# Kernel tuning notes

Hardware: AMD Instinct MI355X
Metric: run time of the kernel (lower is better)

## Reference

```python
import jax, jax.numpy as jnp
import numpy as np

EPS = 1e-8
CG_TOL = 1e-4
S_SIGMA = 8   # bilateral grid spatial downsampling
N_BINS = 9    # bilateral grid range bins (intensity in [0,1])


def _conv2d(x, k):
    # x [C,H,W], k [kh,kw] -> same-padded cross-correlation, per channel
    kh, kw = k.shape
    out = jax.lax.conv_general_dilated(x[:, None], k[None, None], (1, 1),
                                       [(kh // 2, kh // 2), (kw // 2, kw // 2)])
    return out[:, 0]


def _conv2d_T(x, k):
    return _conv2d(x, k[::-1, ::-1])


def _conv_bank(x, ks):
    # x [C,H,W], ks [N,kh,kw] -> [N,C,H,W]
    n, kh, kw = ks.shape
    out = jax.lax.conv_general_dilated(x[:, None], ks[:, None], (1, 1),
                                       [(kh // 2, kh // 2), (kw // 2, kw // 2)])
    return out.transpose(1, 0, 2, 3)


def _conv_bank_T(v, ks):
    # v [N,C,H,W] -> sum_n conv(v[n], flip(ks[n])) : [C,H,W]
    n, kh, kw = ks.shape
    lhs = v.transpose(1, 0, 2, 3)          # [C,N,H,W]
    rhs = ks[:, ::-1, ::-1][None]          # [1,N,kh,kw]
    out = jax.lax.conv_general_dilated(lhs, rhs, (1, 1),
                                       [(kh // 2, kh // 2), (kw // 2, kw // 2)])
    return out[:, 0]


def _deconv_grad(blurred, x, kernel, dkw, dks, rkw, rks, rpow, reg_targets):
    # gradient of E(x) = sum_i dkw_i ||dk_i * (k*x - b)||^2
    #                  + sum_j rkw_j sum |rk_j*x - t_j|^{p_j}
    Kx = _conv2d(x, kernel) - blurred
    d = _conv_bank(Kx, dks)                                    # [Nd,C,H,W]
    g = _conv2d_T(_conv_bank_T(2.0 * dkw[:, None, None, None] * d, dks), kernel)
    v = _conv_bank(x, rks) - reg_targets                       # [Nr,C,H,W]
    av = jnp.abs(v) + EPS
    phi = jnp.sign(v) * av ** (rpow[:, None, None, None] - 1.0)
    g = g + _conv_bank_T(rkw[:, None, None, None] * rpow[:, None, None, None] * phi, rks)
    return g


def _deconv_alpha(blurred, x, kernel, dkw, dks, rkw, rks, rpow, reg_targets, p):
    # exact line search for the quadratic part, Gauss-Newton for |.|^p prior
    g = _deconv_grad(blurred, x, kernel, dkw, dks, rkw, rks, rpow, reg_targets)
    num = -jnp.sum(g * p)
    Kp = _conv2d(p, kernel)
    dKp = _conv_bank(Kp, dks)
    den = jnp.sum(2.0 * dkw[:, None, None, None] * dKp ** 2)
    v = _conv_bank(x, rks) - reg_targets
    Rp = _conv_bank(p, rks)
    w = (rkw * rpow * (rpow - 1.0))[:, None, None, None]
    den = den + jnp.sum(w * (jnp.abs(v) + EPS) ** (rpow[:, None, None, None] - 2.0) * Rp ** 2)
    return num / (den + 1e-12)


def _deconv_prior(x, rks, thr):
    # soft-shrinkage of filtered responses -> regularization targets
    v = _conv_bank(x, rks)
    return jnp.sign(v) * jnp.maximum(jnp.abs(v) - thr[:, None, None, None], 0.0)


def _conv_axis(g, f, axis):
    k = f.shape[0]; r = k // 2; L = g.shape[axis]
    pad = [(0, 0)] * g.ndim; pad[axis] = (r, r)
    gp = jnp.pad(g, pad)
    out = jnp.zeros_like(g)
    for t in range(k):  # fixed small tap count
        out = out + f[t] * jax.lax.slice_in_dim(gp, t, t + L, axis=axis)
    return out


def _bilateral_channel(I, fs, fr):
    # learned-filter bilateral grid: splat -> separable filter (fs,fs,fr) -> trilinear slice
    H, W = I.shape
    gh, gw = H // S_SIGMA, W // S_SIGMA
    Ic = jnp.clip(I, 0.0, 1.0)
    yy, xx = jnp.meshgrid(jnp.arange(H), jnp.arange(W), indexing="ij")
    yi = yy // S_SIGMA; xi = xx // S_SIGMA
    zi = jnp.clip(jnp.round(Ic * (N_BINS - 1)).astype(jnp.int32), 0, N_BINS - 1)
    flat = ((yi * gw + xi) * N_BINS + zi).ravel()
    gv = jnp.zeros(gh * gw * N_BINS, Ic.dtype).at[flat].add(Ic.ravel())
    gw_ = jnp.zeros(gh * gw * N_BINS, Ic.dtype).at[flat].add(1.0)
    g2 = jnp.stack([gv, gw_], -1).reshape(gh, gw, N_BINS, 2)
    g2 = _conv_axis(_conv_axis(_conv_axis(g2, fs, 0), fs, 1), fr, 2)
    yf = yy / S_SIGMA; xf = xx / S_SIGMA; zf = Ic * (N_BINS - 1)

    def corners(f, n):
        c0 = jnp.clip(jnp.floor(f).astype(jnp.int32), 0, n - 1)
        c1 = jnp.minimum(c0 + 1, n - 1)
        w = jnp.clip(f - c0, 0.0, 1.0)
        return c0, c1, w

    y0, y1, wy = corners(yf, gh)
    x0, x1, wx = corners(xf, gw)
    z0, z1, wz = corners(zf, N_BINS)
    acc = jnp.zeros(I.shape + (2,), Ic.dtype)
    for yc, wyc in ((y0, 1 - wy), (y1, wy)):
        for xc, wxc in ((x0, 1 - wx), (x1, wx)):
            for zc, wzc in ((z0, 1 - wz), (z1, wz)):
                acc = acc + (wyc * wxc * wzc)[..., None] * g2[yc, xc, zc]
    return acc[..., 0] / (acc[..., 1] + 1e-8)


def _forward(blurred_batch, kernel_batch, data_kernels, data_kernel_weights,
             reg_kernels, reg_kernel_weights, reg_powers, filter_s, filter_r,
             reg_thresholds, num_cg_iter):
    num_stages = filter_s.shape[0]
    n_reg = reg_kernels.shape[1]

    def single(blurred, kernel):
        def cg(x, idx, reg_targets):
            dkw = data_kernel_weights[idx]; dks = data_kernels[idx]
            rkw = reg_kernel_weights[idx]; rks = reg_kernels[idx]; rp = reg_powers[idx]
            g = _deconv_grad(blurred, x, kernel, dkw, dks, rkw, rks, rp, reg_targets)
            r = -g
            r_norm = jnp.sum(r * r)
            r0 = r_norm

            def body(i, carry):
                x, r, p, rn, done = carry
                alpha = _deconv_alpha(blurred, x, kernel, dkw, dks, rkw, rks, rp, reg_targets, p)
                x1 = x + alpha * p
                g1 = _deconv_grad(blurred, x1, kernel, dkw, dks, rkw, rks, rp, reg_targets)
                r1 = -g1
                nrn = jnp.sum(r1 * r1)
                beta = nrn / (rn + 1e-20)
                conv_now = nrn < CG_TOL * r0
                p1 = r1 + beta * p
                x_n = jnp.where(done, x, x1)
                r_n = jnp.where(done, r, r1)
                rn_n = jnp.where(done, rn, nrn)
                p_n = jnp.where(done | conv_now, p, p1)
                return (x_n, r_n, p_n, rn_n, done | conv_now)

            carry = (x, r, r, r_norm, jnp.array(False))
            x, _, _, _, _ = jax.lax.fori_loop(0, num_cg_iter, body, carry)
            return x

        x = cg(blurred, 0, jnp.zeros((n_reg,) + blurred.shape, blurred.dtype))
        for stage in range(num_stages):
            x = jax.vmap(lambda ch: _bilateral_channel(ch, filter_s[stage], filter_r[stage]))(x)
            reg_targets = _deconv_prior(x, reg_kernels[stage + 1], reg_thresholds[stage])
            x = cg(x, stage + 1, reg_targets)
        return x

    return jax.vmap(single)(blurred_batch, kernel_batch)


def setup_inputs() -> dict:
    key = jax.random.key(0)
    k1, k2 = jax.random.split(key)
    B, C, H, W, KS = 2, 3, 512, 512, 15
    blurred = jax.random.uniform(k1, (B, C, H, W), jnp.float32)
    kern = jax.random.uniform(k2, (B, KS, KS), jnp.float32)
    kern = kern / jnp.sum(kern, axis=(1, 2), keepdims=True)  # normalized PSFs

    ns = 1; c = 2  # num_stages, kernel center (5x5)
    rk = np.zeros((ns + 1, 5, 5, 5), np.float32)
    rk[:, 0, c, c] = -1.0; rk[:, 0, c + 1, c] = 1.0
    rk[:, 1, c, c] = -1.0; rk[:, 1, c, c + 1] = 1.0
    rk[:, 2, c, c] = 1.0; rk[:, 2, c + 1, c] = -1.0
    rk[:, 2, c, c + 1] = -1.0; rk[:, 2, c + 1, c + 1] = 1.0
    rk[:, 3, c - 1, c] = 1.0; rk[:, 3, c, c] = -2.0; rk[:, 3, c + 1, c] = 1.0
    rk[:, 4, c, c - 1] = 1.0; rk[:, 4, c, c] = -2.0; rk[:, 4, c, c + 1] = 1.0
    dk = np.zeros((ns + 1, 6, 5, 5), np.float32)
    dk[:, 0, c, c] = 1.0
    dk[:, 1:] = rk
    dkw = np.zeros((ns + 1, 6), np.float32); dkw[:, 0] = 1.0
    rkw = np.zeros((ns + 1, 5), np.float32)
    rkw[0, :] = 0.001; rkw[1:, :] = 0.05
    rpow = np.full((ns + 1, 5), 2.0, np.float32)
    fs = np.zeros((ns, 11), np.float32); fs[:, 3:8] = [0.0, 1.0, 2.0, 1.0, 0.0]
    fr = np.tile(np.array([0.0, 1.0, 2.0, 1.0, 0.0], np.float32), (ns, 1))
    thr = np.tile(np.array([0.065, 0.065, 0.0325, 0.0325, 0.0325], np.float32), (ns, 1))

    return {
        "blurred_batch": blurred,
        "kernel_batch": kern,
        "data_kernels": jnp.asarray(dk),
        "data_kernel_weights": jnp.asarray(dkw),
        "reg_kernels": jnp.asarray(rk),
        "reg_kernel_weights": jnp.asarray(rkw),
        "reg_powers": jnp.asarray(rpow),
        "filter_s": jnp.asarray(fs),
        "filter_r": jnp.asarray(fr),
        "reg_thresholds": jnp.asarray(thr),
        "num_cg_iter": 5,
    }


def reference(blurred_batch, kernel_batch, data_kernels, data_kernel_weights,
              reg_kernels, reg_kernel_weights, reg_powers, filter_s, filter_r,
              reg_thresholds, num_cg_iter):
    return _forward(blurred_batch, kernel_batch, data_kernels, data_kernel_weights,
                    reg_kernels, reg_kernel_weights, reg_powers, filter_s, filter_r,
                    reg_thresholds, num_cg_iter)
```

## Files before the change

kernel.cpp:

```cpp
#include <hip/hip_runtime.h>

constexpr int Bn = 2, Cn = 3, Hh = 512, Ww = 512;
constexpr int KS = 15, KR = 7;
constexpr int NDK = 6, NRK = 5;
constexpr int GH = 64, GW = 64, NBn = 9, SS = 8;
constexpr float EPSf = 1e-8f;
constexpr float CGTOL = 1e-4f;
constexpr int PLANE = Hh * Ww;
constexpr int CHW = Cn * PLANE;
constexpr int BX = 64, BY = 16;
constexpr int GXc = Ww / BX, GYc = Hh / BY;
constexpr int PB = GXc * GYc * Cn;
constexpr int SA = 80, THt = 30;
constexpr int S2W = 72, S2H = 24;
constexpr int PHW = 68, PHH = 20;
constexpr int PHG = (PHW / 4) * PHH;
constexpr int NITER = 5;

struct CgState { float alpha, beta, rn, r0; int done, pflag; int pad0, pad1; };

__device__ __forceinline__ float blockReduce(float v, float* red, int tid) {
    red[tid] = v; __syncthreads();
    for (int s = 128; s > 0; s >>= 1) { if (tid < s) red[tid] += red[tid + s]; __syncthreads(); }
    float r = red[0]; __syncthreads();
    return r;
}

__global__ __launch_bounds__(256)
void k_conv15(const float* __restrict__ src, const float* __restrict__ rb,
              const float* __restrict__ pbuf, float* __restrict__ xcopy,
              const float* __restrict__ sub, float* __restrict__ out,
              const float* __restrict__ kernB, float* __restrict__ part,
              const CgState* __restrict__ st, const int* __restrict__ ncg,
              int iter, int mode)
{
    const int pz = blockIdx.z, b = pz / Cn, c = pz % Cn;
    const CgState s = st[b];
    if (mode == 2 && (s.done != 0 || iter >= *ncg)) return;
    __shared__ __align__(16) float tile[SA * THt];
    __shared__ __align__(16) float kkp[15 * 16];
    __shared__ float red[256];
    const int tx = threadIdx.x, ty = threadIdx.y, tid = ty * 16 + tx;
    const int ox0 = blockIdx.x * BX, oy0 = blockIdx.y * BY;
    const int baseP = pz * PLANE;
    const float beta = s.beta; const int pf = s.pflag;

    const float* kp = kernB + b * 225;
    for (int i = tid; i < 225; i += 256) kkp[(i / 15) * 16 + (i % 15)] = kp[i];

    float nm = 0.f;
    for (int i = tid; i < 78 * THt; i += 256) {
        int ly = i / 78, lx = i % 78;
        int gy = oy0 - KR + ly, gx = ox0 - KR + lx;
        float v = 0.f;
        if (gy >= 0 && gy < Hh && gx >= 0 && gx < Ww) {
            int gi = baseP + gy * Ww + gx;
            if (mode == 2) {
                float rv = rb[gi], pv = pbuf[gi];
                v = pf ? fmaf(beta, pv, rv) : pv;
                if (ly >= KR && ly < KR + BY && lx >= KR && lx < KR + BX)
                    nm = fmaf(rv, v, nm);
            } else {
                v = src[gi];
                if (mode == 0 && ly >= KR && ly < KR + BY && lx >= KR && lx < KR + BX)
                    xcopy[gi] = v;
            }
        }
        tile[ly * SA + lx] = v;
    }
    __syncthreads();

    const int colbase = tx * 4;
    float a0 = 0.f, a1 = 0.f, a2 = 0.f, a3 = 0.f;
    for (int i = 0; i < KS; i++) {
        const float4* rp4 = reinterpret_cast<const float4*>(&tile[(ty + i) * SA + colbase]);
        float f[20];
        #pragma unroll
        for (int s5 = 0; s5 < 5; s5++) {
            float4 w4 = rp4[s5];
            f[s5 * 4] = w4.x; f[s5 * 4 + 1] = w4.y; f[s5 * 4 + 2] = w4.z; f[s5 * 4 + 3] = w4.w;
        }
        const float4* kr4 = reinterpret_cast<const float4*>(&kkp[i * 16]);
        float kf[16];
        #pragma unroll
        for (int s5 = 0; s5 < 4; s5++) {
            float4 k4 = kr4[s5];
            kf[s5 * 4] = k4.x; kf[s5 * 4 + 1] = k4.y; kf[s5 * 4 + 2] = k4.z; kf[s5 * 4 + 3] = k4.w;
        }
        #pragma unroll
        for (int j = 0; j < KS; j++) {
            float kv = kf[j];
            a0 = fmaf(kv, f[j], a0); a1 = fmaf(kv, f[j + 1], a1);
            a2 = fmaf(kv, f[j + 2], a2); a3 = fmaf(kv, f[j + 3], a3);
        }
    }
    const int gi = baseP + (oy0 + ty) * Ww + ox0 + colbase;
    if (sub) {
        float4 sv = *reinterpret_cast<const float4*>(&sub[gi]);
        a0 -= sv.x; a1 -= sv.y; a2 -= sv.z; a3 -= sv.w;
    }
    *reinterpret_cast<float4*>(&out[gi]) = make_float4(a0, a1, a2, a3);
    if (mode == 2) {
        float tot = blockReduce(nm, red, tid);
        if (tid == 0) {
            int blk = c * (GXc * GYc) + blockIdx.y * GXc + blockIdx.x;
            part[((size_t)b * 4 + 0) * PB + blk] = tot;
        }
    }
}

__global__ __launch_bounds__(256)
void k_bank(const float* __restrict__ sbuf, float* __restrict__ tbuf,
            const float* __restrict__ dks, const float* __restrict__ dkw,
            const CgState* __restrict__ st, const int* __restrict__ ncg,
            int iter, int mode)
{
    const int pz = blockIdx.z, b = pz / Cn;
    if (mode == 1 && (st[b].done != 0 || iter >= *ncg)) return;
    __shared__ __align__(16) float sl[S2W * S2H];
    __shared__ __align__(16) float dl[PHW * PHH];
    __shared__ float dkk[NDK * 25];
    __shared__ float dww[NDK];
    const int tx = threadIdx.x, ty = threadIdx.y, tid = ty * 16 + tx;
    const int ox0 = blockIdx.x * BX, oy0 = blockIdx.y * BY;
    const int baseP = pz * PLANE;
    const int colbase = tx * 4;
    for (int i = tid; i < NDK * 25; i += 256) dkk[i] = dks[i];
    if (tid < NDK) dww[tid] = dkw[tid];
    __syncthreads();

    bool fast = true;
    for (int n = 0; n < NDK; n++) {
        if (dww[n] == 0.f) continue;
        int nnz = 0;
        for (int q = 0; q < 25; q++) if (dkk[n * 25 + q] != 0.f) nnz++;
        if (nnz > 1) fast = false;
    }

    if (fast) {
        const int gy = oy0 + ty, gx0 = ox0 + colbase;
        const float4 sv = *reinterpret_cast<const float4*>(&sbuf[baseP + gy * Ww + gx0]);
        float o0 = 0.f, o1 = 0.f, o2 = 0.f, o3 = 0.f;
        for (int n = 0; n < NDK; n++) {
            float wn = 2.f * dww[n];
            if (wn == 0.f) continue;
            int pa = -1, pb = 0; float pv = 0.f;
            for (int q = 0; q < 25; q++) {
                float vq = dkk[n * 25 + q];
                if (vq != 0.f) { pa = q / 5; pb = q % 5; pv = vq; }
            }
            if (pa < 0) continue;
            int dy = pa - 2, dx = pb - 2;
            float sc = wn * pv * pv;
            if ((gy - dy) < 0 || (gy - dy) >= Hh) continue;
            if ((gx0     - dx) >= 0 && (gx0     - dx) < Ww) o0 = fmaf(sc, sv.x, o0);
            if ((gx0 + 1 - dx) >= 0 && (gx0 + 1 - dx) < Ww) o1 = fmaf(sc, sv.y, o1);
            if ((gx0 + 2 - dx) >= 0 && (gx0 + 2 - dx) < Ww) o2 = fmaf(sc, sv.z, o2);
            if ((gx0 + 3 - dx) >= 0 && (gx0 + 3 - dx) < Ww) o3 = fmaf(sc, sv.w, o3);
        }
        *reinterpret_cast<float4*>(&tbuf[baseP + gy * Ww + gx0]) = make_float4(o0, o1, o2, o3);
        return;
    }

    for (int i = tid; i < S2W * S2H; i += 256) {
        int ly = i / S2W, lx = i % S2W;
        int gy = oy0 - 4 + ly, gx = ox0 - 4 + lx;
        sl[i] = (gy >= 0 && gy < Hh && gx >= 0 && gx < Ww) ? sbuf[baseP + gy * Ww + gx] : 0.f;
    }
    __syncthreads();
    float t0 = 0.f, t1 = 0.f, t2 = 0.f, t3 = 0.f;
    for (int n = 0; n < NDK; n++) {
        float wn = 2.f * dww[n];
        if (wn == 0.f) continue;
        float dnr[25];
        #pragma unroll
        for (int q = 0; q < 25; q++) dnr[q] = dkk[n * 25 + q];
        for (int t = tid; t < PHG; t += 256) {
            int zy = t / 17, zx0 = (t % 17) * 4;
            int gy = oy0 - 2 + zy, gx0 = ox0 - 2 + zx0;
            float v0 = 0.f, v1 = 0.f, v2 = 0.f, v3 = 0.f;
            #pragma unroll
            for (int a = 0; a < 5; a++) {
                bool rz = dnr[a*5]==0.f && dnr[a*5+1]==0.f && dnr[a*5+2]==0.f &&
                          dnr[a*5+3]==0.f && dnr[a*5+4]==0.f;
                if (rz) continue;
                const float4* s4 = reinterpret_cast<const float4*>(&sl[(zy + a) * S2W + zx0]);
                float4 u0 = s4[0], u1 = s4[1];
                float f8[8] = {u0.x,u0.y,u0.z,u0.w,u1.x,u1.y,u1.z,u1.w};
                #pragma unroll
                for (int bb = 0; bb < 5; bb++) {
                    float kv = dnr[a * 5 + bb];
                    if (kv != 0.f) {
                        v0 = fmaf(kv, f8[bb], v0); v1 = fmaf(kv, f8[bb+1], v1);
                        v2 = fmaf(kv, f8[bb+2], v2); v3 = fmaf(kv, f8[bb+3], v3);
                    }
                }
            }
            bool gyin = (gy >= 0 && gy < Hh);
            if (!gyin || gx0     < 0 || gx0     >= Ww) v0 = 0.f;
            if (!gyin || gx0 + 1 < 0 || gx0 + 1 >= Ww) v1 = 0.f;
            if (!gyin || gx0 + 2 < 0 || gx0 + 2 >= Ww) v2 = 0.f;
            if (!gyin || gx0 + 3 < 0 || gx0 + 3 >= Ww) v3 = 0.f;
            *reinterpret_cast<float4*>(&dl[zy * PHW + zx0]) = make_float4(v0, v1, v2, v3);
        }
        __syncthreads();
        float c0 = 0.f, c1 = 0.f, c2 = 0.f, c3 = 0.f;
        #pragma unroll
        for (int a = 0; a < 5; a++) {
            int fr = 4 - a;
            bool rz = dnr[fr*5]==0.f && dnr[fr*5+1]==0.f && dnr[fr*5+2]==0.f &&
                      dnr[fr*5+3]==0.f && dnr[fr*5+4]==0.f;
            if (rz) continue;
            const float4* q4 = reinterpret_cast<const float4*>(&dl[(ty + a) * PHW + colbase]);
            float4 u0 = q4[0], u1 = q4[1];
            float f8[8] = {u0.x,u0.y,u0.z,u0.w,u1.x,u1.y,u1.z,u1.w};
            #pragma unroll
            for (int bb = 0; bb < 5; bb++) {
                float kv = dnr[fr * 5 + (4 - bb)];
                if (kv != 0.f) {
                    c0 = fmaf(kv, f8[bb], c0); c1 = fmaf(kv, f8[bb+1], c1);
                    c2 = fmaf(kv, f8[bb+2], c2); c3 = fmaf(kv, f8[bb+3], c3);
                }
            }
        }
        t0 = fmaf(wn, c0, t0); t1 = fmaf(wn, c1, t1);
        t2 = fmaf(wn, c2, t2); t3 = fmaf(wn, c3, t3);
        __syncthreads();
    }
    const int gi = baseP + (oy0 + ty) * Ww + ox0 + colbase;
    *reinterpret_cast<float4*>(&tbuf[gi]) = make_float4(t0, t1, t2, t3);
}

__global__ __launch_bounds__(256)
void k_grad(const float* __restrict__ wbuf, const float* __restrict__ xg,
            const float* __restrict__ rb, const float* __restrict__ pbuf,
            const float* __restrict__ tgt, float* __restrict__ outb,
            float* __restrict__ pout, const float* __restrict__ kernB,
            const float* __restrict__ rks, const float* __restrict__ rkw,
            const float* __restrict__ rpw, float* __restrict__ part,
            const CgState* __restrict__ st, const int* __restrict__ ncg,
            int iter, int mode)
{
    const int pz = blockIdx.z, b = pz / Cn, c = pz % Cn;
    const CgState s = st[b];
    if (mode == 1 && (s.done != 0 || iter >= *ncg)) return;
    __shared__ __align__(16) float wt[SA * THt];
    __shared__ __align__(16) float s2[S2W * S2H];
    __shared__ __align__(16) float ph[PHW * PHH];
    __shared__ __align__(16) float kkp[15 * 16];
    __shared__ float rk5[NRK * 25];
    __shared__ float srkw[NRK], srpw[NRK];
    __shared__ float red[256];
    const int tx = threadIdx.x, ty = threadIdx.y, tid = ty * 16 + tx;
    const int ox0 = blockIdx.x * BX, oy0 = blockIdx.y * BY;
    const int baseP = pz * PLANE;
    const float beta = s.beta; const int pf = s.pflag;

    const float* kp = kernB + b * 225;
    for (int i = tid; i < 225; i += 256) kkp[(i / 15) * 16 + (i % 15)] = kp[224 - i];
    for (int i = tid; i < NRK * 25; i += 256) rk5[i] = rks[i];
    if (tid < NRK) { srkw[tid] = rkw[tid]; srpw[tid] = rpw[tid]; }

    for (int i = tid; i < 78 * THt; i += 256) {
        int ly = i / 78, lx = i % 78;
        int gy = oy0 - KR + ly, gx = ox0 - KR + lx;
        wt[ly * SA + lx] = (gy >= 0 && gy < Hh && gx >= 0 && gx < Ww)
                           ? wbuf[baseP + gy * Ww + gx] : 0.f;
    }
    for (int i = tid; i < S2W * S2H; i += 256) {
        int ly = i / S2W, lx = i % S2W;
        int gy = oy0 - 4 + ly, gx = ox0 - 4 + lx;
        float v = 0.f;
        if (gy >= 0 && gy < Hh && gx >= 0 && gx < Ww) {
            int gi = baseP + gy * Ww + gx;
            if (mode == 0) v = xg[gi];
            else { float rv = rb[gi], pv = pbuf[gi]; v = pf ? fmaf(beta, pv, rv) : pv; }
        }
        s2[i] = v;
    }
    __syncthreads();

    const int colbase = tx * 4;
    float a0 = 0.f, a1 = 0.f, a2 = 0.f, a3 = 0.f;
    for (int i = 0; i < KS; i++) {
        const float4* rp4 = reinterpret_cast<const float4*>(&wt[(ty + i) * SA + colbase]);
        float f[20];
        #pragma unroll
        for (int s5 = 0; s5 < 5; s5++) {
            float4 w4 = rp4[s5];
            f[s5 * 4] = w4.x; f[s5 * 4 + 1] = w4.y; f[s5 * 4 + 2] = w4.z; f[s5 * 4 + 3] = w4.w;
        }
        const float4* kr4 = reinterpret_cast<const float4*>(&kkp[i * 16]);
        float kf[16];
        #pragma unroll
        for (int s5 = 0; s5 < 4; s5++) {
            float4 k4 = kr4[s5];
            kf[s5 * 4] = k4.x; kf[s5 * 4 + 1] = k4.y; kf[s5 * 4 + 2] = k4.z; kf[s5 * 4 + 3] = k4.w;
        }
        #pragma unroll
        for (int j = 0; j < KS; j++) {
            float kv = kf[j];
            a0 = fmaf(kv, f[j], a0); a1 = fmaf(kv, f[j + 1], a1);
            a2 = fmaf(kv, f[j + 2], a2); a3 = fmaf(kv, f[j + 3], a3);
        }
    }

    for (int m = 0; m < NRK; m++) {
        float wm = srkw[m], rp = srpw[m];
        if (wm == 0.f) continue;
        float rmr[25];
        #pragma unroll
        for (int q = 0; q < 25; q++) rmr[q] = rk5[m * 25 + q];
        const float* tgm = tgt ? tgt + ((size_t)(b * NRK + m)) * CHW + (size_t)c * PLANE : nullptr;
        const float coefG = wm * rp;
        const float coefH = wm * rp * (rp - 1.f);

        for (int t = tid; t < PHG; t += 256) {
            int zy = t / 17, zx0 = (t % 17) * 4;
            int gy = oy0 - 2 + zy, gx0 = ox0 - 2 + zx0;
            float v0 = 0.f, v1 = 0.f, v2 = 0.f, v3 = 0.f;
            #pragma unroll
            for (int a = 0; a < 5; a++) {
                bool rz = rmr[a*5]==0.f && rmr[a*5+1]==0.f && rmr[a*5+2]==0.f &&
                          rmr[a*5+3]==0.f && rmr[a*5+4]==0.f;
                if (rz) continue;
                const float4* s4 = reinterpret_cast<const float4*>(&s2[(zy + a) * S2W + zx0]);
                float4 u0 = s4[0], u1 = s4[1];
                float f8[8] = {u0.x,u0.y,u0.z,u0.w,u1.x,u1.y,u1.z,u1.w};
                #pragma unroll
                for (int bb = 0; bb < 5; bb++) {
                    float kv = rmr[a * 5 + bb];
                    if (kv != 0.f) {
                        v0 = fmaf(kv, f8[bb], v0); v1 = fmaf(kv, f8[bb+1], v1);
                        v2 = fmaf(kv, f8[bb+2], v2); v3 = fmaf(kv, f8[bb+3], v3);
                    }
                }
            }
            bool gyin = (gy >= 0 && gy < Hh);
            float o0 = 0.f, o1 = 0.f, o2 = 0.f, o3 = 0.f;
            if (mode == 0) {
                if (gyin && gx0     >= 0 && gx0     < Ww) {
                    float v = v0; if (tgm) v -= tgm[gy * Ww + gx0];
                    float sg = (v > 0.f) ? 1.f : ((v < 0.f) ? -1.f : 0.f);
                    float av = fabsf(v) + EPSf;
                    o0 = coefG * sg * ((rp == 2.f) ? av : powf(av, rp - 1.f));
                }
                if (gyin && gx0 + 1 >= 0 && gx0 + 1 < Ww) {
                    float v = v1; if (tgm) v -= tgm[gy * Ww + gx0 + 1];
                    float sg = (v > 0.f) ? 1.f : ((v < 0.f) ? -1.f : 0.f);
                    float av = fabsf(v) + EPSf;
                    o1 = coefG * sg * ((rp == 2.f) ? av : powf(av, rp - 1.f));
                }
                if (gyin && gx0 + 2 >= 0 && gx0 + 2 < Ww) {
                    float v = v2; if (tgm) v -= tgm[gy * Ww + gx0 + 2];
                    float sg = (v > 0.f) ? 1.f : ((v < 0.f) ? -1.f : 0.f);
                    float av = fabsf(v) + EPSf;
                    o2 = coefG * sg * ((rp == 2.f) ? av : powf(av, rp - 1.f));
                }
                if (gyin && gx0 + 3 >= 0 && gx0 + 3 < Ww) {
                    float v = v3; if (tgm) v -= tgm[gy * Ww + gx0 + 3];
                    float sg = (v > 0.f) ? 1.f : ((v < 0.f) ? -1.f : 0.f);
                    float av = fabsf(v) + EPSf;
                    o3 = coefG * sg * ((rp == 2.f) ? av : powf(av, rp - 1.f));
                }
            } else {
                #pragma unroll
                for (int j = 0; j < 4; j++) {
                    int gx = gx0 + j;
                    if (!gyin || gx < 0 || gx >= Ww) continue;
                    float v = (j == 0) ? v0 : (j == 1) ? v1 : (j == 2) ? v2 : v3;
                    float fac = 1.f;
                    if (rp != 2.f) {
                        float vx = 0.f;
                        for (int a = 0; a < 5; a++)
                            for (int bb = 0; bb < 5; bb++) {
                                int yy = gy - 2 + a, xx = gx - 2 + bb;
                                if (yy >= 0 && yy < Hh && xx >= 0 && xx < Ww)
                                    vx = fmaf(rmr[a * 5 + bb], xg[baseP + yy * Ww + xx], vx);
                            }
                        if (tgm) vx -= tgm[gy * Ww + gx];
                        fac = powf(fabsf(vx) + EPSf, rp - 2.f);
                    }
                    float o = coefH * fac * v;
                    if (j == 0) o0 = o; else if (j == 1) o1 = o; else if (j == 2) o2 = o; else o3 = o;
                }
            }
            *reinterpret_cast<float4*>(&ph[zy * PHW + zx0]) = make_float4(o0, o1, o2, o3);
        }
        __syncthreads();
        #pragma unroll
        for (int a = 0; a < 5; a++) {
            int fr = 4 - a;
            bool rz = rmr[fr*5]==0.f && rmr[fr*5+1]==0.f && rmr[fr*5+2]==0.f &&
                      rmr[fr*5+3]==0.f && rmr[fr*5+4]==0.f;
            if (rz) continue;
            const float4* q4 = reinterpret_cast<const float4*>(&ph[(ty + a) * PHW + colbase]);
            float4 u0 = q4[0], u1 = q4[1];
            float f8[8] = {u0.x,u0.y,u0.z,u0.w,u1.x,u1.y,u1.z,u1.w};
            #pragma unroll
            for (int bb = 0; bb < 5; bb++) {
                float kv = rmr[fr * 5 + (4 - bb)];
                if (kv != 0.f) {
                    a0 = fmaf(kv, f8[bb], a0); a1 = fmaf(kv, f8[bb+1], a1);
                    a2 = fmaf(kv, f8[bb+2], a2); a3 = fmaf(kv, f8[bb+3], a3);
                }
            }
        }
        __syncthreads();
    }

    const int gi = baseP + (oy0 + ty) * Ww + ox0 + colbase;
    float redv;
    if (mode == 0) {
        float r0v = -a0, r1v = -a1, r2v = -a2, r3v = -a3;
        float4 rv4 = make_float4(r0v, r1v, r2v, r3v);
        *reinterpret_cast<float4*>(&outb[gi]) = rv4;
        *reinterpret_cast<float4*>(&pout[gi]) = rv4;
        redv = r0v * r0v + r1v * r1v + r2v * r2v + r3v * r3v;
    } else {
        *reinterpret_cast<float4*>(&outb[gi]) = make_float4(a0, a1, a2, a3);
        int li = (ty + 4) * S2W + colbase + 4;
        redv = s2[li] * a0 + s2[li + 1] * a1 + s2[li + 2] * a2 + s2[li + 3] * a3;
    }
    float tot = blockReduce(redv, red, tid);
    if (tid == 0) {
        int blk = c * (GXc * GYc) + blockIdx.y * GXc + blockIdx.x;
        int slot = (mode == 0) ? 2 : 1;
        part[((size_t)b * 4 + slot) * PB + blk] = tot;
    }
}

__global__ __launch_bounds__(256)
void k_axpy(float4* __restrict__ x, float4* __restrict__ r, float4* __restrict__ p,
            const float4* __restrict__ q, float* __restrict__ part,
            const CgState* __restrict__ st, const int* __restrict__ ncg, int iter)
{
    const int b = blockIdx.y;
    const CgState s = st[b];
    if (s.done != 0 || iter >= *ncg) return;
    __shared__ float red[256];
    const int tid = threadIdx.x;
    const int idx = b * (CHW / 4) + blockIdx.x * 256 + tid;
    float4 pv = p[idx], rv = r[idx], qv = q[idx], xv = x[idx];
    float4 pc;
    if (s.pflag) {
        pc.x = fmaf(s.beta, pv.x, rv.x); pc.y = fmaf(s.beta, pv.y, rv.y);
        pc.z = fmaf(s.beta, pv.z, rv.z); pc.w = fmaf(s.beta, pv.w, rv.w);
    } else pc = pv;
    xv.x = fmaf(s.alpha, pc.x, xv.x); xv.y = fmaf(s.alpha, pc.y, xv.y);
    xv.z = fmaf(s.alpha, pc.z, xv.z); xv.w = fmaf(s.alpha, pc.w, xv.w);
    rv.x = fmaf(-s.alpha, qv.x, rv.x); rv.y = fmaf(-s.alpha, qv.y, rv.y);
    rv.z = fmaf(-s.alpha, qv.z, rv.z); rv.w = fmaf(-s.alpha, qv.w, rv.w);
    x[idx] = xv; r[idx] = rv; p[idx] = pc;
    float nr = rv.x * rv.x + rv.y * rv.y + rv.z * rv.z + rv.w * rv.w;
    float tot = blockReduce(nr, red, tid);
    if (tid == 0) part[((size_t)b * 4 + 2) * PB + blockIdx.x] = tot;
}

__global__ __launch_bounds__(256)
void k_fin_alpha(const float* __restrict__ part, CgState* st,
                 const int* __restrict__ ncg, int iter)
{
    const int b = blockIdx.x, tid = threadIdx.x;
    __shared__ float red[256];
    if (st[b].done != 0 || iter >= *ncg) { if (tid == 0) st[b].alpha = 0.f; return; }
    float sn = 0.f, sd = 0.f;
    for (int i = tid; i < PB; i += 256) {
        sn += part[((size_t)b * 4 + 0) * PB + i];
        sd += part[((size_t)b * 4 + 1) * PB + i];
    }
    float num = blockReduce(sn, red, tid);
    float den = blockReduce(sd, red, tid);
    if (tid == 0) st[b].alpha = num / (den + 1e-12f);
}

__global__ __launch_bounds__(256)
void k_fin_iter(const float* __restrict__ part, CgState* st,
                const int* __restrict__ ncg, int iter, int mode)
{
    const int b = blockIdx.x, tid = threadIdx.x;
    __shared__ float red[256];
    if (mode == 1 && (st[b].done != 0 || iter >= *ncg)) { if (tid == 0) st[b].pflag = 0; return; }
    float s = 0.f;
    for (int i = tid; i < PB; i += 256) s += part[((size_t)b * 4 + 2) * PB + i];
    float nrn = blockReduce(s, red, tid);
    if (tid == 0) {
        if (mode == 0) {
            st[b].rn = nrn; st[b].r0 = nrn; st[b].done = 0; st[b].pflag = 0;
            st[b].beta = 0.f; st[b].alpha = 0.f;
        } else {
            float beta = nrn / (st[b].rn + 1e-20f);
            int conv = (nrn < CGTOL * st[b].r0) ? 1 : 0;
            st[b].beta = beta; st[b].rn = nrn;
            st[b].pflag = conv ? 0 : 1;
            if (conv) st[b].done = 1;
        }
    }
}

__global__ __launch_bounds__(64)
void k_splat(const float* __restrict__ x, float* __restrict__ grid)
{
    __shared__ float bins[NBn * 2];
    const int tid = threadIdx.y * 8 + threadIdx.x;
    if (tid < NBn * 2) bins[tid] = 0.f;
    __syncthreads();
    const int pz = blockIdx.z;
    const int gy = blockIdx.y, gx = blockIdx.x;
    const int py = gy * 8 + threadIdx.y, px = gx * 8 + threadIdx.x;
    float I = x[(size_t)pz * PLANE + py * Ww + px];
    float Ic = fminf(fmaxf(I, 0.f), 1.f);
    int zi = (int)rintf(Ic * (NBn - 1));
    zi = min(max(zi, 0), NBn - 1);
    atomicAdd(&bins[zi * 2], Ic);
    atomicAdd(&bins[zi * 2 + 1], 1.f);
    __syncthreads();
    if (tid < NBn * 2)
        grid[(size_t)pz * GH * GW * NBn * 2 + ((size_t)gy * GW + gx) * NBn * 2 + tid] = bins[tid];
}

__global__ __launch_bounds__(256)
void k_blur(const float* __restrict__ in, float* __restrict__ out,
            const float* __restrict__ taps, int ntaps, int axis)
{
    const int id = blockIdx.x * 256 + threadIdx.x;
    const int total = Bn * Cn * GH * GW * NBn;
    if (id >= total) return;
    const int z = id % NBn;
    const int x = (id / NBn) % GW;
    const int y = (id / (NBn * GW)) % GH;
    const int p = id / (NBn * GW * GH);
    int coord, lim; long stride;
    if (axis == 0)      { coord = y; lim = GH;  stride = (long)GW * NBn * 2; }
    else if (axis == 1) { coord = x; lim = GW;  stride = NBn * 2; }
    else                { coord = z; lim = NBn; stride = 2; }
    const long base = (((long)(p * GH + y) * GW + x) * NBn + z) * 2;
    const int r = ntaps / 2;
    float a0 = 0.f, a1 = 0.f;
    for (int t = 0; t < ntaps; t++) {
        int cc = coord + t - r;
        if (cc < 0 || cc >= lim) continue;
        float w = taps[t];
        long ofs = base + (long)(cc - coord) * stride;
        a0 = fmaf(w, in[ofs], a0);
        a1 = fmaf(w, in[ofs + 1], a1);
    }
    out[base] = a0; out[base + 1] = a1;
}

__global__ __launch_bounds__(256)
void k_slice(const float* __restrict__ xin, const float* __restrict__ grid,
             float* __restrict__ xout)
{
    const int pz = blockIdx.z;
    const int id = blockIdx.x * 256 + threadIdx.x;
    const int py = id / Ww, px = id % Ww;
    float I = xin[(size_t)pz * PLANE + id];
    float Ic = fminf(fmaxf(I, 0.f), 1.f);
    float yf = (float)py / SS, xf = (float)px / SS, zf = Ic * (NBn - 1);
    int y0 = min(max((int)floorf(yf), 0), GH - 1); int y1 = min(y0 + 1, GH - 1);
    float wy = fminf(fmaxf(yf - (float)y0, 0.f), 1.f);
    int x0 = min(max((int)floorf(xf), 0), GW - 1); int x1 = min(x0 + 1, GW - 1);
    float wx = fminf(fmaxf(xf - (float)x0, 0.f), 1.f);
    int z0 = min(max((int)floorf(zf), 0), NBn - 1); int z1 = min(z0 + 1, NBn - 1);
    float wz = fminf(fmaxf(zf - (float)z0, 0.f), 1.f);
    const float* gp = grid + (size_t)pz * GH * GW * NBn * 2;
    const int   ys[2] = { y0, y1 };  const float wys[2] = { 1.f - wy, wy };
    const int   xs[2] = { x0, x1 };  const float wxs[2] = { 1.f - wx, wx };
    const int   zs[2] = { z0, z1 };  const float wzs[2] = { 1.f - wz, wz };
    float a0 = 0.f, a1 = 0.f;
    for (int iy = 0; iy < 2; iy++)
        for (int ix = 0; ix < 2; ix++)
            for (int iz = 0; iz < 2; iz++) {
                float w = wys[iy] * wxs[ix] * wzs[iz];
                size_t idx = (((size_t)ys[iy] * GW + xs[ix]) * NBn + zs[iz]) * 2;
                a0 = fmaf(w, gp[idx], a0);
                a1 = fmaf(w, gp[idx + 1], a1);
            }
    xout[(size_t)pz * PLANE + id] = a0 / (a1 + 1e-8f);
}

__global__ __launch_bounds__(256)
void k_prior(const float* __restrict__ x, float* __restrict__ tgt,
             const float* __restrict__ rks, const float* __restrict__ thr)
{
    const int pz = blockIdx.z, b = pz / Cn, c = pz % Cn;
    __shared__ float xl[24 * 24];
    __shared__ float rkk[NRK * 25];
    __shared__ float sthr[NRK];
    const int tx = threadIdx.x, ty = threadIdx.y, tid = ty * 16 + tx;
    const int ox0 = blockIdx.x * 16, oy0 = blockIdx.y * 16;
    const int baseP = pz * PLANE;
    for (int i = tid; i < NRK * 25; i += 256) rkk[i] = rks[i];
    if (tid < NRK) sthr[tid] = thr[tid];
    for (int i = tid; i < 24 * 24; i += 256) {
        int ly = i / 24, lx = i % 24;
        int gy = oy0 - 2 + ly, gx = ox0 - 2 + lx;
        xl[i] = (gy >= 0 && gy < Hh && gx >= 0 && gx < Ww) ? x[baseP + gy * Ww + gx] : 0.f;
    }
    __syncthreads();
    const int pix = (oy0 + ty) * Ww + (ox0 + tx);
    for (int m = 0; m < NRK; m++) {
        const float* rm = &rkk[m * 25];
        float v = 0.f;
        #pragma unroll
        for (int a = 0; a < 5; a++)
            #pragma unroll
            for (int bb = 0; bb < 5; bb++)
                v = fmaf(rm[a * 5 + bb], xl[(ty + a) * 24 + (tx + bb)], v);
        float sg = (v > 0.f) ? 1.f : ((v < 0.f) ? -1.f : 0.f);
        tgt[((size_t)(b * NRK + m)) * CHW + (size_t)c * PLANE + pix] =
            sg * fmaxf(fabsf(v) - sthr[m], 0.f);
    }
}

extern "C" void kernel_launch(void* const* d_in, const int* in_sizes, int n_in,
                              void* d_out, int out_size, void* d_ws, size_t ws_size,
                              hipStream_t stream)
{
    const float* blurred = (const float*)d_in[0];
    const float* kern    = (const float*)d_in[1];
    const float* dks     = (const float*)d_in[2];
    const float* dkw     = (const float*)d_in[3];
    const float* rks     = (const float*)d_in[4];
    const float* rkw     = (const float*)d_in[5];
    const float* rpw     = (const float*)d_in[6];
    const float* fs      = (const float*)d_in[7];
    const float* fr      = (const float*)d_in[8];
    const float* thr     = (const float*)d_in[9];
    const int*   ncg     = (const int*)d_in[10];
    (void)in_sizes; (void)n_in; (void)out_size; (void)ws_size;

    float* w = (float*)d_ws;
    size_t off = 0;
    auto alloc = [&](size_t n) { float* p = w + off; off += n; return p; };
    float* xb   = alloc((size_t)Bn * CHW);
    float* pbuf = alloc((size_t)Bn * CHW);
    float* rbuf = alloc((size_t)Bn * CHW);
    float* kx   = alloc((size_t)Bn * CHW);
    float* wb   = alloc((size_t)Bn * CHW);
    float* qb   = alloc((size_t)Bn * CHW);
    float* tg   = alloc((size_t)Bn * NRK * CHW);
    float* g0   = alloc((size_t)Bn * Cn * GH * GW * NBn * 2);
    float* g1   = alloc((size_t)Bn * Cn * GH * GW * NBn * 2);
    float* part = alloc((size_t)Bn * 4 * PB);
    CgState* st = (CgState*)(w + off); off += Bn * 8;

    dim3 tb(16, 16), grd(GXc, GYc, Bn * Cn);

    auto solve = [&](int idx, const float* tgt, int initmode) {
        const float* dks_i = dks + (size_t)idx * NDK * 25;
        const float* dkw_i = dkw + (size_t)idx * NDK;
        const float* rks_i = rks + (size_t)idx * NRK * 25;
        const float* rkw_i = rkw + (size_t)idx * NRK;
        const float* rpw_i = rpw + (size_t)idx * NRK;
        k_conv15<<<grd, tb, 0, stream>>>(initmode == 0 ? blurred : xb, nullptr, nullptr,
                                         initmode == 0 ? xb : nullptr, blurred, kx, kern,
                                         nullptr, st, ncg, 0, initmode == 0 ? 0 : 1);
        k_bank<<<grd, tb, 0, stream>>>(kx, wb, dks_i, dkw_i, st, ncg, 0, 0);
        k_grad<<<grd, tb, 0, stream>>>(wb, xb, nullptr, nullptr, tgt, rbuf, pbuf, kern,
                                       rks_i, rkw_i, rpw_i, part, st, ncg, 0, 0);
        k_fin_iter<<<Bn, 256, 0, stream>>>(part, st, ncg, 0, 0);
        for (int i = 0; i < NITER; i++) {
            k_conv15<<<grd, tb, 0, stream>>>(nullptr, rbuf, pbuf, nullptr, nullptr, kx, kern,
                                             part, st, ncg, i, 2);
            k_bank<<<grd, tb, 0, stream>>>(kx, wb, dks_i, dkw_i, st, ncg, i, 1);
            k_grad<<<grd, tb, 0, stream>>>(wb, xb, rbuf, pbuf, tgt, qb, nullptr, kern,
                                           rks_i, rkw_i, rpw_i, part, st, ncg, i, 1);
            k_fin_alpha<<<Bn, 256, 0, stream>>>(part, st, ncg, i);
            k_axpy<<<dim3(PB, Bn), 256, 0, stream>>>((float4*)xb, (float4*)rbuf, (float4*)pbuf,
                                                     (const float4*)qb, part, st, ncg, i);
            k_fin_iter<<<Bn, 256, 0, stream>>>(part, st, ncg, i, 1);
        }
    };

    solve(0, nullptr, 0);

    dim3 sb(8, 8), sg(GW, GH, Bn * Cn);
    k_splat<<<sg, sb, 0, stream>>>(xb, g0);
    const int totalg = Bn * Cn * GH * GW * NBn;
    k_blur<<<(totalg + 255) / 256, 256, 0, stream>>>(g0, g1, fs, 11, 0);
    k_blur<<<(totalg + 255) / 256, 256, 0, stream>>>(g1, g0, fs, 11, 1);
    k_blur<<<(totalg + 255) / 256, 256, 0, stream>>>(g0, g1, fr, 5, 2);
    k_slice<<<dim3(PLANE / 256, 1, Bn * Cn), 256, 0, stream>>>(xb, g1, xb);

    k_prior<<<dim3(Ww / 16, Hh / 16, Bn * Cn), tb, 0, stream>>>(xb, tg, rks + NRK * 25, thr);

    solve(1, tg, 1);

    hipMemcpyAsync(d_out, xb, (size_t)Bn * CHW * sizeof(float),
                   hipMemcpyDeviceToDevice, stream);
}
```

Before: 1.565 ms.

## Fold single-tap data bank into conv and collapse p=2 prior into 9x9 stencil

A setup kernel precomputes per-solve info. When every data kernel has a single nonzero tap, the bank scaling is folded into the conv15 output and k_bank exits early. When all regularizer powers are 2, the prior Hessian R^T W R is collapsed into one precomputed 9x9 stencil applied in a new k_hess kernel, replacing the generic gradient/Hessian path in CG iterations. This removes a full-image pass and the two-stage bank convolution per iteration, at the cost of slower exact boundary handling and extra kernel launches that exit early.

```diff
diff --git a/kernel.cpp b/kernel.cpp
--- a/kernel.cpp
+++ b/kernel.cpp
@@ -19,6 +19,17 @@
 
 struct CgState { float alpha, beta, rn, r0; int done, pflag; int pad0, pad1; };
 
+struct SolveInfo {
+    int fastBank;
+    int allrp2;
+    int nd;
+    int pad;
+    float sctot;
+    float dsc[NDK];
+    int ddy[NDK], ddx[NDK];
+    float C[81];
+};
+
 __device__ __forceinline__ float blockReduce(float v, float* red, int tid) {
     red[tid] = v; __syncthreads();
     for (int s = 128; s > 0; s >>= 1) { if (tid < s) red[tid] += red[tid + s]; __syncthreads(); }
@@ -26,11 +37,67 @@
     return r;
 }
 
+__global__ __launch_bounds__(128)
+void k_comp(const float* __restrict__ dkw, const float* __restrict__ dks,
+            const float* __restrict__ rkw, const float* __restrict__ rpw,
+            const float* __restrict__ rks, SolveInfo* si)
+{
+    const int idx = blockIdx.x;
+    SolveInfo* s = si + idx;
+    const float* dkw_i = dkw + idx * NDK;
+    const float* dks_i = dks + (size_t)idx * NDK * 25;
+    const float* rkw_i = rkw + idx * NRK;
+    const float* rpw_i = rpw + idx * NRK;
+    const float* rks_i = rks + (size_t)idx * NRK * 25;
+    const int t = threadIdx.x;
+    if (t < 81) {
+        int oy = t / 9 - 4, ox = t % 9 - 4;
+        float acc = 0.f;
+        for (int m = 0; m < NRK; m++) {
+            float wm = rkw_i[m], rp = rpw_i[m];
+            float ch = wm * rp * (rp - 1.f);
+            if (ch == 0.f) continue;
+            for (int ay = 0; ay < 5; ay++)
+                for (int ax = 0; ax < 5; ax++) {
+                    int by = ay - oy, bx = ax - ox;
+                    if (by < 0 || by >= 5 || bx < 0 || bx >= 5) continue;
+                    acc += ch * rks_i[m * 25 + ay * 5 + ax] * rks_i[m * 25 + by * 5 + bx];
+                }
+        }
+        s->C[t] = acc;
+    }
+    if (t == 81) {
+        int fast = 1, nd = 0; float tot = 0.f;
+        for (int n = 0; n < NDK; n++) {
+            if (dkw_i[n] == 0.f) continue;
+            int cnt = 0, pos = -1;
+            for (int q = 0; q < 25; q++) if (dks_i[n * 25 + q] != 0.f) { cnt++; pos = q; }
+            if (cnt > 1) fast = 0;
+            if (cnt == 1 && nd < NDK) {
+                float v = dks_i[n * 25 + pos];
+                s->dsc[nd] = 2.f * dkw_i[n] * v * v;
+                s->ddy[nd] = pos / 5 - 2; s->ddx[nd] = pos % 5 - 2;
+                tot += s->dsc[nd]; nd++;
+            }
+        }
+        s->fastBank = fast; s->nd = fast ? nd : 0; s->sctot = tot;
+    }
+    if (t == 82) {
+        int ok = 1;
+        for (int m = 0; m < NRK; m++) {
+            float wm = rkw_i[m], rp = rpw_i[m];
+            if (wm != 0.f && rp != 2.f && wm * rp * (rp - 1.f) != 0.f) ok = 0;
+        }
+        s->allrp2 = ok;
+    }
+}
+
 __global__ __launch_bounds__(256)
 void k_conv15(const float* __restrict__ src, const float* __restrict__ rb,
               const float* __restrict__ pbuf, float* __restrict__ xcopy,
               const float* __restrict__ sub, float* __restrict__ out,
               const float* __restrict__ kernB, float* __restrict__ part,
+              const SolveInfo* __restrict__ si,
               const CgState* __restrict__ st, const int* __restrict__ ncg,
               int iter, int mode)
 {
@@ -99,6 +166,25 @@
         float4 sv = *reinterpret_cast<const float4*>(&sub[gi]);
         a0 -= sv.x; a1 -= sv.y; a2 -= sv.z; a3 -= sv.w;
     }
+    if (si->fastBank) {
+        const int gy = oy0 + ty, gx0 = ox0 + colbase;
+        if (gy >= 2 && gy <= Hh - 3 && gx0 >= 2 && gx0 + 3 <= Ww - 3) {
+            float sc = si->sctot;
+            a0 *= sc; a1 *= sc; a2 *= sc; a3 *= sc;
+        } else {
+            float m0 = 0.f, m1 = 0.f, m2 = 0.f, m3 = 0.f;
+            int ndl = si->nd;
+            for (int n = 0; n < ndl; n++) {
+                float sc = si->dsc[n]; int dy = si->ddy[n], dx = si->ddx[n];
+                if (gy - dy < 0 || gy - dy >= Hh) continue;
+                if (gx0     - dx >= 0 && gx0     - dx < Ww) m0 += sc;
+                if (gx0 + 1 - dx >= 0 && gx0 + 1 - dx < Ww) m1 += sc;
+                if (gx0 + 2 - dx >= 0 && gx0 + 2 - dx < Ww) m2 += sc;
+                if (gx0 + 3 - dx >= 0 && gx0 + 3 - dx < Ww) m3 += sc;
+            }
+            a0 *= m0; a1 *= m1; a2 *= m2; a3 *= m3;
+        }
+    }
     *reinterpret_cast<float4*>(&out[gi]) = make_float4(a0, a1, a2, a3);
     if (mode == 2) {
         float tot = blockReduce(nm, red, tid);
@@ -112,9 +198,11 @@
 __global__ __launch_bounds__(256)
 void k_bank(const float* __restrict__ sbuf, float* __restrict__ tbuf,
             const float* __restrict__ dks, const float* __restrict__ dkw,
+            const SolveInfo* __restrict__ si,
             const CgState* __restrict__ st, const int* __restrict__ ncg,
             int iter, int mode)
 {
+    if (si->fastBank) return;
     const int pz = blockIdx.z, b = pz / Cn;
     if (mode == 1 && (st[b].done != 0 || iter >= *ncg)) return;
     __shared__ __align__(16) float sl[S2W * S2H];
@@ -127,41 +215,6 @@
     const int colbase = tx * 4;
     for (int i = tid; i < NDK * 25; i += 256) dkk[i] = dks[i];
     if (tid < NDK) dww[tid] = dkw[tid];
-    __syncthreads();
-
-    bool fast = true;
-    for (int n = 0; n < NDK; n++) {
-        if (dww[n] == 0.f) continue;
-        int nnz = 0;
-        for (int q = 0; q < 25; q++) if (dkk[n * 25 + q] != 0.f) nnz++;
-        if (nnz > 1) fast = false;
-    }
-
-    if (fast) {
-        const int gy = oy0 + ty, gx0 = ox0 + colbase;
-        const float4 sv = *reinterpret_cast<const float4*>(&sbuf[baseP + gy * Ww + gx0]);
-        float o0 = 0.f, o1 = 0.f, o2 = 0.f, o3 = 0.f;
-        for (int n = 0; n < NDK; n++) {
-            float wn = 2.f * dww[n];
-            if (wn == 0.f) continue;
-            int pa = -1, pb = 0; float pv = 0.f;
-            for (int q = 0; q < 25; q++) {
-                float vq = dkk[n * 25 + q];
-                if (vq != 0.f) { pa = q / 5; pb = q % 5; pv = vq; }
-            }
-            if (pa < 0) continue;
-            int dy = pa - 2, dx = pb - 2;
-            float sc = wn * pv * pv;
-            if ((gy - dy) < 0 || (gy - dy) >= Hh) continue;
-            if ((gx0     - dx) >= 0 && (gx0     - dx) < Ww) o0 = fmaf(sc, sv.x, o0);
-            if ((gx0 + 1 - dx) >= 0 && (gx0 + 1 - dx) < Ww) o1 = fmaf(sc, sv.y, o1);
-            if ((gx0 + 2 - dx) >= 0 && (gx0 + 2 - dx) < Ww) o2 = fmaf(sc, sv.z, o2);
-            if ((gx0 + 3 - dx) >= 0 && (gx0 + 3 - dx) < Ww) o3 = fmaf(sc, sv.w, o3);
-        }
-        *reinterpret_cast<float4*>(&tbuf[baseP + gy * Ww + gx0]) = make_float4(o0, o1, o2, o3);
-        return;
-    }
-
     for (int i = tid; i < S2W * S2H; i += 256) {
         int ly = i / S2W, lx = i % S2W;
         int gy = oy0 - 4 + ly, gx = ox0 - 4 + lx;
@@ -232,15 +285,155 @@
 }
 
 __global__ __launch_bounds__(256)
-void k_grad(const float* __restrict__ wbuf, const float* __restrict__ xg,
+void k_hess(const float* __restrict__ kx, const float* __restrict__ wb,
             const float* __restrict__ rb, const float* __restrict__ pbuf,
-            const float* __restrict__ tgt, float* __restrict__ outb,
-            float* __restrict__ pout, const float* __restrict__ kernB,
+            float* __restrict__ qb, const float* __restrict__ kernB,
             const float* __restrict__ rks, const float* __restrict__ rkw,
-            const float* __restrict__ rpw, float* __restrict__ part,
-            const CgState* __restrict__ st, const int* __restrict__ ncg,
-            int iter, int mode)
-{
+            const float* __restrict__ rpw, const SolveInfo* __restrict__ si,
+            float* __restrict__ part, const CgState* __restrict__ st,
+            const int* __restrict__ ncg, int iter)
+{
+    if (!si->allrp2) return;
+    const int pz = blockIdx.z, b = pz / Cn, c = pz % Cn;
+    const CgState s = st[b];
+    if (s.done != 0 || iter >= *ncg) return;
+    __shared__ __align__(16) float wt[SA * THt];
+    __shared__ __align__(16) float s2[S2W * S2H];
+    __shared__ __align__(16) float kkp[15 * 16];
+    __shared__ __align__(16) float sC[81];
+    __shared__ float rk5[NRK * 25];
+    __shared__ float srkw[NRK], srpw[NRK];
+    __shared__ float red[256];
+    const int tx = threadIdx.x, ty = threadIdx.y, tid = ty * 16 + tx;
+    const int ox0 = blockIdx.x * BX, oy0 = blockIdx.y * BY;
+    const int baseP = pz * PLANE;
+    const float beta = s.beta; const int pf = s.pflag;
+    const float* wsrc = si->fastBank ? kx : wb;
+
+    const float* kp = kernB + b * 225;
+    for (int i = tid; i < 225; i += 256) kkp[(i / 15) * 16 + (i % 15)] = kp[224 - i];
+    for (int i = tid; i < 81; i += 256) sC[i] = si->C[i];
+    for (int i = tid; i < NRK * 25; i += 256) rk5[i] = rks[i];
+    if (tid < NRK) { srkw[tid] = rkw[tid]; srpw[tid] = rpw[tid]; }
+
+    for (int i = tid; i < 78 * THt; i += 256) {
+        int ly = i / 78, lx = i % 78;
+        int gy = oy0 - KR + ly, gx = ox0 - KR + lx;
+        wt[ly * SA + lx] = (gy >= 0 && gy < Hh && gx >= 0 && gx < Ww)
+                           ? wsrc[baseP + gy * Ww + gx] : 0.f;
+    }
+    for (int i = tid; i < S2W * S2H; i += 256) {
+        int ly = i / S2W, lx = i % S2W;
+        int gy = oy0 - 4 + ly, gx = ox0 - 4 + lx;
+        float v = 0.f;
+        if (gy >= 0 && gy < Hh && gx >= 0 && gx < Ww) {
+            int gi = baseP + gy * Ww + gx;
+            float rv = rb[gi], pv = pbuf[gi];
+            v = pf ? fmaf(beta, pv, rv) : pv;
+        }
+        s2[i] = v;
+    }
+    __syncthreads();
+
+    const int colbase = tx * 4;
+    float a0 = 0.f, a1 = 0.f, a2 = 0.f, a3 = 0.f;
+    for (int i = 0; i < KS; i++) {
+        const float4* rp4 = reinterpret_cast<const float4*>(&wt[(ty + i) * SA + colbase]);
+        float f[20];
+        #pragma unroll
+        for (int s5 = 0; s5 < 5; s5++) {
+            float4 w4 = rp4[s5];
+            f[s5 * 4] = w4.x; f[s5 * 4 + 1] = w4.y; f[s5 * 4 + 2] = w4.z; f[s5 * 4 + 3] = w4.w;
+        }
+        const float4* kr4 = reinterpret_cast<const float4*>(&kkp[i * 16]);
+        float kf[16];
+        #pragma unroll
+        for (int s5 = 0; s5 < 4; s5++) {
+            float4 k4 = kr4[s5];
+            kf[s5 * 4] = k4.x; kf[s5 * 4 + 1] = k4.y; kf[s5 * 4 + 2] = k4.z; kf[s5 * 4 + 3] = k4.w;
+        }
+        #pragma unroll
+        for (int j = 0; j < KS; j++) {
+            float kv = kf[j];
+            a0 = fmaf(kv, f[j], a0); a1 = fmaf(kv, f[j + 1], a1);
+            a2 = fmaf(kv, f[j + 2], a2); a3 = fmaf(kv, f[j + 3], a3);
+        }
+    }
+
+    const int gy = oy0 + ty, gx0 = ox0 + colbase;
+    const bool intr = (gy >= 2 && gy <= Hh - 3 && gx0 >= 2 && gx0 + 3 <= Ww - 3);
+    if (intr) {
+        #pragma unroll
+        for (int oy = 0; oy < 9; oy++) {
+            float cr[9]; bool nz = false;
+            #pragma unroll
+            for (int ox = 0; ox < 9; ox++) { cr[ox] = sC[oy * 9 + ox]; nz = nz || (cr[ox] != 0.f); }
+            if (!nz) continue;
+            const float4* s4 = reinterpret_cast<const float4*>(&s2[(ty + oy) * S2W + colbase]);
+            float4 u0 = s4[0], u1 = s4[1], u2 = s4[2];
+            float f12[12] = {u0.x,u0.y,u0.z,u0.w,u1.x,u1.y,u1.z,u1.w,u2.x,u2.y,u2.z,u2.w};
+            #pragma unroll
+            for (int ox = 0; ox < 9; ox++) {
+                float kv = cr[ox];
+                if (kv != 0.f) {
+                    a0 = fmaf(kv, f12[ox], a0); a1 = fmaf(kv, f12[ox + 1], a1);
+                    a2 = fmaf(kv, f12[ox + 2], a2); a3 = fmaf(kv, f12[ox + 3], a3);
+                }
+            }
+        }
+    } else {
+        #pragma unroll
+        for (int j = 0; j < 4; j++) {
+            int gx = gx0 + j;
+            float acc = 0.f;
+            for (int m = 0; m < NRK; m++) {
+                float wm = srkw[m]; if (wm == 0.f) continue;
+                float rp = srpw[m]; float ch = wm * rp * (rp - 1.f);
+                if (ch == 0.f) continue;
+                for (int by = 0; by < 5; by++)
+                    for (int bx = 0; bx < 5; bx++) {
+                        float kb = rk5[m * 25 + by * 5 + bx];
+                        if (kb == 0.f) continue;
+                        int iy = gy + 2 - by, ix = gx + 2 - bx;
+                        if (iy < 0 || iy >= Hh || ix < 0 || ix >= Ww) continue;
+                        float inner = 0.f;
+                        for (int ay = 0; ay < 5; ay++)
+                            for (int ax = 0; ax < 5; ax++) {
+                                float ka = rk5[m * 25 + ay * 5 + ax];
+                                if (ka != 0.f)
+                                    inner = fmaf(ka, s2[(ty + 4 + ay - by) * S2W + colbase + 4 + j + ax - bx], inner);
+                            }
+                        acc = fmaf(ch * kb, inner, acc);
+                    }
+            }
+            if (j == 0) a0 += acc; else if (j == 1) a1 += acc;
+            else if (j == 2) a2 += acc; else a3 += acc;
+        }
+    }
+
+    const int gi = baseP + gy * Ww + gx0;
+    *reinterpret_cast<float4*>(&qb[gi]) = make_float4(a0, a1, a2, a3);
+    int li = (ty + 4) * S2W + colbase + 4;
+    float redv = s2[li] * a0 + s2[li + 1] * a1 + s2[li + 2] * a2 + s2[li + 3] * a3;
+    float tot = blockReduce(redv, red, tid);
+    if (tid == 0) {
+        int blk = c * (GXc * GYc) + blockIdx.y * GXc + blockIdx.x;
+        part[((size_t)b * 4 + 1) * PB + blk] = tot;
+    }
+}
+
+__global__ __launch_bounds__(256)
+void k_gradL(const float* __restrict__ kx, const float* __restrict__ wb,
+             const float* __restrict__ xg,
+             const float* __restrict__ rb, const float* __restrict__ pbuf,
+             const float* __restrict__ tgt, float* __restrict__ outb,
+             float* __restrict__ pout, const float* __restrict__ kernB,
+             const float* __restrict__ rks, const float* __restrict__ rkw,
+             const float* __restrict__ rpw, const SolveInfo* __restrict__ si,
+             float* __restrict__ part, const CgState* __restrict__ st,
+             const int* __restrict__ ncg, int iter, int mode)
+{
+    if (mode == 1 && si->allrp2) return;
     const int pz = blockIdx.z, b = pz / Cn, c = pz % Cn;
     const CgState s = st[b];
     if (mode == 1 && (s.done != 0 || iter >= *ncg)) return;
@@ -255,6 +448,7 @@
     const int ox0 = blockIdx.x * BX, oy0 = blockIdx.y * BY;
     const int baseP = pz * PLANE;
     const float beta = s.beta; const int pf = s.pflag;
+    const float* wsrc = si->fastBank ? kx : wb;
 
     const float* kp = kernB + b * 225;
     for (int i = tid; i < 225; i += 256) kkp[(i / 15) * 16 + (i % 15)] = kp[224 - i];
@@ -265,7 +459,7 @@
         int ly = i / 78, lx = i % 78;
         int gy = oy0 - KR + ly, gx = ox0 - KR + lx;
         wt[ly * SA + lx] = (gy >= 0 && gy < Hh && gx >= 0 && gx < Ww)
-                           ? wbuf[baseP + gy * Ww + gx] : 0.f;
+                           ? wsrc[baseP + gy * Ww + gx] : 0.f;
     }
     for (int i = tid; i < S2W * S2H; i += 256) {
         int ly = i / S2W, lx = i % S2W;
@@ -338,37 +532,18 @@
             }
             bool gyin = (gy >= 0 && gy < Hh);
             float o0 = 0.f, o1 = 0.f, o2 = 0.f, o3 = 0.f;
-            if (mode == 0) {
-                if (gyin && gx0     >= 0 && gx0     < Ww) {
-                    float v = v0; if (tgm) v -= tgm[gy * Ww + gx0];
+            #pragma unroll
+            for (int j = 0; j < 4; j++) {
+                int gx = gx0 + j;
+                if (!gyin || gx < 0 || gx >= Ww) continue;
+                float v = (j == 0) ? v0 : (j == 1) ? v1 : (j == 2) ? v2 : v3;
+                float o;
+                if (mode == 0) {
+                    if (tgm) v -= tgm[gy * Ww + gx];
                     float sg = (v > 0.f) ? 1.f : ((v < 0.f) ? -1.f : 0.f);
                     float av = fabsf(v) + EPSf;
-                    o0 = coefG * sg * ((rp == 2.f) ? av : powf(av, rp - 1.f));
-                }
-                if (gyin && gx0 + 1 >= 0 && gx0 + 1 < Ww) {
-                    float v = v1; if (tgm) v -= tgm[gy * Ww + gx0 + 1];
-                    float sg = (v > 0.f) ? 1.f : ((v < 0.f) ? -1.f : 0.f);
-                    float av = fabsf(v) + EPSf;
-                    o1 = coefG * sg * ((rp == 2.f) ? av : powf(av, rp - 1.f));
-                }
-                if (gyin && gx0 + 2 >= 0 && gx0 + 2 < Ww) {
-                    float v = v2; if (tgm) v -= tgm[gy * Ww + gx0 + 2];
-                    float sg = (v > 0.f) ? 1.f : ((v < 0.f) ? -1.f : 0.f);
-                    float av = fabsf(v) + EPSf;
-                    o2 = coefG * sg * ((rp == 2.f) ? av : powf(av, rp - 1.f));
-                }
-                if (gyin && gx0 + 3 >= 0 && gx0 + 3 < Ww) {
-                    float v = v3; if (tgm) v -= tgm[gy * Ww + gx0 + 3];
-                    float sg = (v > 0.f) ? 1.f : ((v < 0.f) ? -1.f : 0.f);
-                    float av = fabsf(v) + EPSf;
-                    o3 = coefG * sg * ((rp == 2.f) ? av : powf(av, rp - 1.f));
-                }
-            } else {
-                #pragma unroll
-                for (int j = 0; j < 4; j++) {
-                    int gx = gx0 + j;
-                    if (!gyin || gx < 0 || gx >= Ww) continue;
-                    float v = (j == 0) ? v0 : (j == 1) ? v1 : (j == 2) ? v2 : v3;
+                    o = coefG * sg * ((rp == 2.f) ? av : powf(av, rp - 1.f));
+                } else {
                     float fac = 1.f;
                     if (rp != 2.f) {
                         float vx = 0.f;
@@ -381,9 +556,9 @@
                         if (tgm) vx -= tgm[gy * Ww + gx];
                         fac = powf(fabsf(vx) + EPSf, rp - 2.f);
                     }
-                    float o = coefH * fac * v;
-                    if (j == 0) o0 = o; else if (j == 1) o1 = o; else if (j == 2) o2 = o; else o3 = o;
+                    o = coefH * fac * v;
                 }
+                if (j == 0) o0 = o; else if (j == 1) o1 = o; else if (j == 2) o2 = o; else o3 = o;
             }
             *reinterpret_cast<float4*>(&ph[zy * PHW + zx0]) = make_float4(o0, o1, o2, o3);
         }
@@ -645,8 +820,11 @@
     float* g1   = alloc((size_t)Bn * Cn * GH * GW * NBn * 2);
     float* part = alloc((size_t)Bn * 4 * PB);
     CgState* st = (CgState*)(w + off); off += Bn * 8;
+    SolveInfo* sinf = (SolveInfo*)(w + off); off += 2 * ((sizeof(SolveInfo) + 3) / 4);
 
     dim3 tb(16, 16), grd(GXc, GYc, Bn * Cn);
+
+    k_comp<<<2, 128, 0, stream>>>(dkw, dks, rkw, rpw, rks, sinf);
 
     auto solve = [&](int idx, const float* tgt, int initmode) {
         const float* dks_i = dks + (size_t)idx * NDK * 25;
@@ -654,19 +832,22 @@
         const float* rks_i = rks + (size_t)idx * NRK * 25;
         const float* rkw_i = rkw + (size_t)idx * NRK;
         const float* rpw_i = rpw + (size_t)idx * NRK;
+        const SolveInfo* si = sinf + idx;
         k_conv15<<<grd, tb, 0, stream>>>(initmode == 0 ? blurred : xb, nullptr, nullptr,
                                          initmode == 0 ? xb : nullptr, blurred, kx, kern,
-                                         nullptr, st, ncg, 0, initmode == 0 ? 0 : 1);
-        k_bank<<<grd, tb, 0, stream>>>(kx, wb, dks_i, dkw_i, st, ncg, 0, 0);
-        k_grad<<<grd, tb, 0, stream>>>(wb, xb, nullptr, nullptr, tgt, rbuf, pbuf, kern,
-                                       rks_i, rkw_i, rpw_i, part, st, ncg, 0, 0);
+                                         nullptr, si, st, ncg, 0, initmode == 0 ? 0 : 3);
+        k_bank<<<grd, tb, 0, stream>>>(kx, wb, dks_i, dkw_i, si, st, ncg, 0, 0);
+        k_gradL<<<grd, tb, 0, stream>>>(kx, wb, xb, nullptr, nullptr, tgt, rbuf, pbuf, kern,
+                                        rks_i, rkw_i, rpw_i, si, part, st, ncg, 0, 0);
         k_fin_iter<<<Bn, 256, 0, stream>>>(part, st, ncg, 0, 0);
         for (int i = 0; i < NITER; i++) {
             k_conv15<<<grd, tb, 0, stream>>>(nullptr, rbuf, pbuf, nullptr, nullptr, kx, kern,
-                                             part, st, ncg, i, 2);
-            k_bank<<<grd, tb, 0, stream>>>(kx, wb, dks_i, dkw_i, st, ncg, i, 1);
-            k_grad<<<grd, tb, 0, stream>>>(wb, xb, rbuf, pbuf, tgt, qb, nullptr, kern,
-                                           rks_i, rkw_i, rpw_i, part, st, ncg, i, 1);
+                                             part, si, st, ncg, i, 2);
+            k_bank<<<grd, tb, 0, stream>>>(kx, wb, dks_i, dkw_i, si, st, ncg, i, 1);
+            k_hess<<<grd, tb, 0, stream>>>(kx, wb, rbuf, pbuf, qb, kern,
+                                           rks_i, rkw_i, rpw_i, si, part, st, ncg, i);
+            k_gradL<<<grd, tb, 0, stream>>>(kx, wb, xb, rbuf, pbuf, tgt, qb, nullptr, kern,
+                                            rks_i, rkw_i, rpw_i, si, part, st, ncg, i, 1);
             k_fin_alpha<<<Bn, 256, 0, stream>>>(part, st, ncg, i);
             k_axpy<<<dim3(PB, Bn), 256, 0, stream>>>((float4*)xb, (float4*)rbuf, (float4*)pbuf,
                                                      (const float4*)qb, part, st, ncg, i);
```

Result: slower. 2.311 ms (+47.7%).
